# Kernel tuning notes

Measured on AMD Instinct MI355X. Metric: run time of the kernel, lower is better.

Reference implementation:

```python
import jax, jax.numpy as jnp
import numpy as np

D, H, HK, DH = 2048, 32, 8, 64
RQ = RKV = 48
RO = RFF = 1024
INTER = 8192
B, T = 2, 1024
THETA = 10000.0
EPS = 1e-5
NEG = -1e30


def _rms(x, w):
    v = jnp.mean(x * x, axis=-1, keepdims=True)
    return x * jax.lax.rsqrt(v + EPS) * w


def _proj_per_head(x, Us, V):
    # x:[B,T,D], V:[h,r,D], Us:[h,dh,r] -> [B,h,T,dh]
    xr = jnp.einsum('btd,hrd->bthr', x, V)
    return jnp.einsum('bthr,hdr->bhtd', xr, Us)


def _rope_cos_sin(position_ids, dh):
    inv = 1.0 / (THETA ** (jnp.arange(0, dh, 2, dtype=jnp.float32) / dh))
    ang = position_ids.astype(jnp.float32)[:, None] * inv[None, :]   # [T, dh/2]
    ang = jnp.repeat(ang, 2, axis=-1)                                # interleaved, per source
    return jnp.cos(ang), jnp.sin(ang)                                # [T, dh]


def _rotate_half(x):
    d = x.shape[-1] // 2
    return jnp.concatenate([-x[..., d:], x[..., :d]], axis=-1)


def setup_inputs() -> dict:
    key = jax.random.key(0)
    ks = jax.random.split(key, 18)
    g = lambda i, shape, s: (jax.random.normal(ks[i], shape, jnp.float32) * s)
    return {
        'x': g(0, (B, T, D), 1.0),
        'position_ids': jnp.arange(T, dtype=jnp.int32),
        'ln1_w': jnp.ones((D,), jnp.float32),
        'ln2_w': jnp.ones((D,), jnp.float32),
        'q_Us': g(1, (H, DH, RQ), 0.05), 'q_V': g(2, (H, RQ, D), 0.05),
        'k_Us': g(3, (HK, DH, RKV), 0.05), 'k_V': g(4, (HK, RKV, D), 0.05),
        'v_Us': g(5, (HK, DH, RKV), 0.05), 'v_V': g(6, (HK, RKV, D), 0.05),
        'o_Us': g(7, (D, RO), 0.02), 'o_V': g(8, (RO, H * DH), 0.02),
        'g_Us': g(9, (INTER, RFF), 0.02), 'g_V': g(10, (RFF, D), 0.02),
        'u_Us': g(11, (INTER, RFF), 0.02), 'u_V': g(12, (RFF, D), 0.02),
        'd_Us': g(13, (D, RFF), 0.02), 'd_V': g(14, (RFF, INTER), 0.02),
    }


def reference(x, position_ids, ln1_w, ln2_w,
              q_Us, q_V, k_Us, k_V, v_Us, v_V,
              o_Us, o_V, g_Us, g_V, u_Us, u_V, d_Us, d_V):
    Bx, Tx, Dx = x.shape
    n_rep = H // HK

    # ---- attention sub-block ----
    h = _rms(x, ln1_w)
    q = _proj_per_head(h, q_Us, q_V)          # [B,H,T,dh]
    k = _proj_per_head(h, k_Us, k_V)          # [B,Hk,T,dh]
    v = _proj_per_head(h, v_Us, v_V)          # [B,Hk,T,dh]

    cos, sin = _rope_cos_sin(position_ids, DH)          # [T,dh]
    cos = cos[None, None]; sin = sin[None, None]
    q = q * cos + _rotate_half(q) * sin
    k = k * cos + _rotate_half(k) * sin

    k = jnp.repeat(k, n_rep, axis=1)          # GQA expand -> [B,H,T,dh]
    v = jnp.repeat(v, n_rep, axis=1)

    scale = 1.0 / jnp.sqrt(jnp.float32(DH))
    scores = jnp.einsum('bhtd,bhsd->bhts', q, k) * scale
    causal = jnp.tril(jnp.ones((Tx, Tx), bool))
    scores = jnp.where(causal[None, None], scores, NEG)
    p = jax.nn.softmax(scores, axis=-1)
    attn = jnp.einsum('bhts,bhsd->bhtd', p, v)            # [B,H,T,dh]
    attn = attn.transpose(0, 2, 1, 3).reshape(Bx, Tx, H * DH)

    # low-rank o projection: W_o ~= o_Us @ o_V
    ar = jnp.einsum('btk,rk->btr', attn, o_V)
    attn_out = jnp.einsum('btr,dr->btd', ar, o_Us)
    x = x + attn_out

    # ---- low-rank SwiGLU MLP ----
    h2 = _rms(x, ln2_w)
    gate = jnp.einsum('btr,ir->bti', jnp.einsum('btd,rd->btr', h2, g_V), g_Us)
    up = jnp.einsum('btr,ir->bti', jnp.einsum('btd,rd->btr', h2, u_V), u_Us)
    inner = jax.nn.silu(gate) * up
    down = jnp.einsum('btr,dr->btd', jnp.einsum('bti,ri->btr', inner, d_V), d_Us)
    return x + down
```

## Files before the change

kernel.cpp:

```cpp
#include <hip/hip_runtime.h>

typedef unsigned short u16;
typedef unsigned int u32;
typedef unsigned long long u64;

typedef __bf16 bf16x8 __attribute__((ext_vector_type(8)));
typedef float f32x4 __attribute__((ext_vector_type(4)));

__device__ __forceinline__ float bf2f(u16 u) {
  union { u32 i; float f; } v; v.i = ((u32)u) << 16; return v.f;
}
__device__ __forceinline__ u16 f2bf(float f) {
  union { float f; u32 i; } v; v.f = f;
  u32 r = v.i + 0x7fff + ((v.i >> 16) & 1);
  return (u16)(r >> 16);
}
__device__ __forceinline__ u32 packbf(float a, float b) {
  return (u32)f2bf(a) | ((u32)f2bf(b) << 16);
}

__device__ __forceinline__ void gload_lds16(const u16* g, u16* l) {
  __builtin_amdgcn_global_load_lds(
      (const __attribute__((address_space(1))) void*)g,
      (__attribute__((address_space(3))) void*)l, 16, 0, 0);
}

__global__ void detect_k(const u32* __restrict__ w, u32* __restrict__ flag) {
  if (threadIdx.x == 0 && blockIdx.x == 0)
    *flag = (w[0] == 0x3F803F80u) ? 0u : 1u;
}

struct CvtTab {
  const void* src[16];
  u64 doff[16];
  u32 bstart[16];
};

__global__ __launch_bounds__(256)
void convert_k(CvtTab tab, u16* __restrict__ wbase, const u32* __restrict__ dflag)
{
  const u32 f = *dflag;
  const int blk = blockIdx.x;
  int t = 15;
#pragma unroll
  for (int i = 15; i >= 1; i--) if (blk < (int)tab.bstart[i]) t = i - 1;
  const u64 eoff = (u64)(blk - tab.bstart[t]) * 2048 + threadIdx.x * 8;
  u16* dst = wbase + tab.doff[t] + eoff;
  if (f == 0) {
    uint4 v = *(const uint4*)((const u16*)tab.src[t] + eoff);
    *(uint4*)dst = v;
  } else {
    const float* s = (const float*)tab.src[t] + eoff;
    uint4 lo = *(const uint4*)s;
    uint4 hi = *(const uint4*)(s + 4);
    union { u32 i; float fv; } c0,c1,c2,c3,c4,c5,c6,c7;
    c0.i = lo.x; c1.i = lo.y; c2.i = lo.z; c3.i = lo.w;
    c4.i = hi.x; c5.i = hi.y; c6.i = hi.z; c7.i = hi.w;
    uint4 pb;
    pb.x = packbf(c0.fv, c1.fv); pb.y = packbf(c2.fv, c3.fv);
    pb.z = packbf(c4.fv, c5.fv); pb.w = packbf(c6.fv, c7.fv);
    *(uint4*)dst = pb;
  }
}

template<int EPI, int TILE, int BK>
__global__ __launch_bounds__(256)
void gemm_bt(const u16* __restrict__ A, const u16* __restrict__ B,
             void* Cout, const void* R,
             int K, int lda, int ldc, int pstride, const u32* __restrict__ dflag)
{
  constexpr int WT = TILE / 2;
  constexpr int NF = TILE / 32;
  constexpr int CH = BK / 8;
  constexpr int ITER_S = TILE * CH / 256;
  __shared__ u16 sA[TILE * BK];
  __shared__ u16 sB[TILE * BK];
  const u32 f = *dflag;
  const int tid  = threadIdx.x;
  const int bm   = blockIdx.y * TILE;
  const int bn   = blockIdx.x * TILE;
  const int Klen = K / gridDim.z;
  const int kbase = blockIdx.z * Klen;
  const int wave = tid >> 6, lane = tid & 63;
  const int wm = (wave >> 1) * WT, wn = (wave & 1) * WT;
  const int lr = lane & 15, lq = lane >> 4;

  f32x4 acc[NF][NF];
#pragma unroll
  for (int i = 0; i < NF; i++)
#pragma unroll
    for (int j = 0; j < NF; j++) { f32x4 z = {0.f,0.f,0.f,0.f}; acc[i][j] = z; }

  int scA[ITER_S], scRow[ITER_S];
#pragma unroll
  for (int j = 0; j < ITER_S; j++) {
    int s = (wave * ITER_S + j) * 64 + lane;
    scRow[j] = s / CH;
    scA[j] = (((s % CH)) ^ (scRow[j] & 7)) * 8;
  }

  for (int k0 = kbase; k0 < kbase + Klen; k0 += BK) {
#pragma unroll
    for (int j = 0; j < ITER_S; j++) {
      const u16* ga = A + (size_t)(bm + scRow[j]) * lda + k0 + scA[j];
      const u16* gb = B + (size_t)(bn + scRow[j]) * K + k0 + scA[j];
      gload_lds16(ga, &sA[(wave * ITER_S + j) * 512]);
      gload_lds16(gb, &sB[(wave * ITER_S + j) * 512]);
    }
    __syncthreads();
#pragma unroll
    for (int kk = 0; kk < BK; kk += 32) {
      bf16x8 af[NF], bfr[NF];
#pragma unroll
      for (int i = 0; i < NF; i++)
        af[i] = *(const bf16x8*)
            &sA[(wm + i * 16 + lr) * BK + ((((kk >> 3) + lq) ^ (lr & 7)) * 8)];
#pragma unroll
      for (int i = 0; i < NF; i++)
        bfr[i] = *(const bf16x8*)
            &sB[(wn + i * 16 + lr) * BK + ((((kk >> 3) + lq) ^ (lr & 7)) * 8)];
#pragma unroll
      for (int i = 0; i < NF; i++)
#pragma unroll
        for (int j = 0; j < NF; j++)
          acc[i][j] = __builtin_amdgcn_mfma_f32_16x16x32_bf16(af[i], bfr[j], acc[i][j], 0, 0, 0);
    }
    __syncthreads();
  }

  u16* outz = (u16*)Cout + (size_t)blockIdx.z * pstride;
#pragma unroll
  for (int i = 0; i < NF; i++) {
#pragma unroll
    for (int j = 0; j < NF; j++) {
#pragma unroll
      for (int e = 0; e < 4; e++) {
        int row = bm + wm + i * 16 + lq * 4 + e;
        int col = bn + wn + j * 16 + lr;
        size_t idx = (size_t)row * ldc + col;
        float v = acc[i][j][e];
        if (EPI == 0) {
          outz[idx] = f2bf(v);
        } else if (EPI == 1) {
          float rv = f ? ((const float*)R)[idx] : bf2f(((const u16*)R)[idx]);
          ((float*)Cout)[idx] = v + rv;
        } else if (EPI == 2) {
          float s = v + ((const float*)R)[idx];
          if (f) ((float*)Cout)[idx] = s;
          else   ((u16*)Cout)[idx] = f2bf(s);
        }
      }
    }
  }
}

__global__ __launch_bounds__(256)
void gemm_gu(const u16* __restrict__ A, const u16* __restrict__ Bg,
             const u16* __restrict__ Bu, u16* __restrict__ Cout,
             int K, int lda, int ldc)
{
  constexpr int TILE = 128, BK = 64, NF = 4, CH = 8, ITER_S = 4;
  __shared__ u16 sA[TILE * BK];
  __shared__ u16 sB[TILE * BK];
  const int tid  = threadIdx.x;
  const int bm   = blockIdx.y * TILE;
  const int bn   = blockIdx.x * TILE;
  const int wave = tid >> 6, lane = tid & 63;
  const int wm = (wave >> 1) * 64, wn = (wave & 1) * 64;
  const int lr = lane & 15, lq = lane >> 4;

  f32x4 accG[NF][NF], accU[NF][NF];
#pragma unroll
  for (int i = 0; i < NF; i++)
#pragma unroll
    for (int j = 0; j < NF; j++) {
      f32x4 z = {0.f,0.f,0.f,0.f}; accG[i][j] = z; accU[i][j] = z;
    }

  int scA[ITER_S], scRow[ITER_S];
#pragma unroll
  for (int j = 0; j < ITER_S; j++) {
    int s = (wave * ITER_S + j) * 64 + lane;
    scRow[j] = s / CH;
    scA[j] = ((s % CH) ^ (scRow[j] & 7)) * 8;
  }

#pragma unroll
  for (int ph = 0; ph < 2; ph++) {
    const u16* Ap = A + (ph ? 1024 : 0);
    const u16* Bp = ph ? Bu : Bg;
    for (int k0 = 0; k0 < K; k0 += BK) {
#pragma unroll
      for (int j = 0; j < ITER_S; j++) {
        gload_lds16(Ap + (size_t)(bm + scRow[j]) * lda + k0 + scA[j],
                    &sA[(wave * ITER_S + j) * 512]);
        gload_lds16(Bp + (size_t)(bn + scRow[j]) * K + k0 + scA[j],
                    &sB[(wave * ITER_S + j) * 512]);
      }
      __syncthreads();
#pragma unroll
      for (int kk = 0; kk < BK; kk += 32) {
        bf16x8 af[NF], bfr[NF];
#pragma unroll
        for (int i = 0; i < NF; i++)
          af[i] = *(const bf16x8*)
              &sA[(wm + i * 16 + lr) * BK + ((((kk >> 3) + lq) ^ (lr & 7)) * 8)];
#pragma unroll
        for (int i = 0; i < NF; i++)
          bfr[i] = *(const bf16x8*)
              &sB[(wn + i * 16 + lr) * BK + ((((kk >> 3) + lq) ^ (lr & 7)) * 8)];
        if (ph == 0) {
#pragma unroll
          for (int i = 0; i < NF; i++)
#pragma unroll
            for (int j = 0; j < NF; j++)
              accG[i][j] = __builtin_amdgcn_mfma_f32_16x16x32_bf16(af[i], bfr[j], accG[i][j], 0, 0, 0);
        } else {
#pragma unroll
          for (int i = 0; i < NF; i++)
#pragma unroll
            for (int j = 0; j < NF; j++)
              accU[i][j] = __builtin_amdgcn_mfma_f32_16x16x32_bf16(af[i], bfr[j], accU[i][j], 0, 0, 0);
        }
      }
      __syncthreads();
    }
  }

#pragma unroll
  for (int i = 0; i < NF; i++) {
#pragma unroll
    for (int j = 0; j < NF; j++) {
#pragma unroll
      for (int e = 0; e < 4; e++) {
        int row = bm + wm + i * 16 + lq * 4 + e;
        int col = bn + wn + j * 16 + lr;
        float g = accG[i][j][e];
        float inner = g / (1.f + __expf(-g)) * accU[i][j][e];
        Cout[(size_t)row * ldc + col] = f2bf(inner);
      }
    }
  }
}

__global__ __launch_bounds__(256)
void reduce2_k(const u16* __restrict__ p, u16* __restrict__ out, int nel)
{
  size_t i = ((size_t)blockIdx.x * 256 + threadIdx.x) * 8;
  uint4 a = *(const uint4*)(p + i);
  uint4 b = *(const uint4*)(p + (size_t)nel + i);
  u32 aa[4] = {a.x, a.y, a.z, a.w};
  u32 bb[4] = {b.x, b.y, b.z, b.w};
  u32 rr[4];
#pragma unroll
  for (int k = 0; k < 4; k++) {
    float s0 = bf2f((u16)aa[k]) + bf2f((u16)bb[k]);
    float s1 = bf2f((u16)(aa[k] >> 16)) + bf2f((u16)(bb[k] >> 16));
    rr[k] = packbf(s0, s1);
  }
  uint4 o; o.x = rr[0]; o.y = rr[1]; o.z = rr[2]; o.w = rr[3];
  *(uint4*)(out + i) = o;
}

template<int XSRC>
__global__ __launch_bounds__(256)
void rmsnorm_k(const void* __restrict__ xin, const u16* __restrict__ w,
               u16* __restrict__ out, const u32* __restrict__ dflag)
{
  const u32 f = *dflag;
  const int n = blockIdx.x, tid = threadIdx.x;
  float v[8]; float ss = 0.f;
#pragma unroll
  for (int i = 0; i < 8; i++) {
    int d = i * 256 + tid;
    float xv;
    if (XSRC == 1)      xv = ((const float*)xin)[(size_t)n * 2048 + d];
    else if (f)         xv = ((const float*)xin)[(size_t)n * 2048 + d];
    else                xv = bf2f(((const u16*)xin)[(size_t)n * 2048 + d]);
    v[i] = xv; ss += xv * xv;
  }
#pragma unroll
  for (int o = 32; o >= 1; o >>= 1) ss += __shfl_xor(ss, o, 64);
  __shared__ float red[4];
  if ((tid & 63) == 0) red[tid >> 6] = ss;
  __syncthreads();
  float tot = red[0] + red[1] + red[2] + red[3];
  float rms = rsqrtf(tot * (1.f / 2048.f) + 1e-5f);
#pragma unroll
  for (int i = 0; i < 8; i++) {
    int d = i * 256 + tid;
    out[(size_t)n * 2048 + d] = f2bf(v[i] * rms * bf2f(w[d]));
  }
}

template<int ROPE, int TRANS>
__global__ __launch_bounds__(256)
void qkv2_k(const u16* __restrict__ xr, const u16* __restrict__ Us,
            const int* __restrict__ pos, u16* __restrict__ out, int NH, int XS)
{
  const int h = blockIdx.y;
  const int tid = threadIdx.x;
  const int n = blockIdx.x * 8 + (tid >> 5);
  const int j = tid & 31;
  const u16* xrow = xr + (size_t)n * XS + h * 48;
  const u16* U = Us + (size_t)h * 64 * 48;
  float a = 0.f, b = 0.f;
#pragma unroll
  for (int r = 0; r < 48; r++) {
    float xv = bf2f(xrow[r]);
    a += xv * bf2f(U[j * 48 + r]);
    b += xv * bf2f(U[(j + 32) * 48 + r]);
  }
  const int t = n & 1023, bb = n >> 10;
  float olo, ohi;
  if (ROPE) {
    float p = (float)pos[t];
    float inv_lo = powf(10000.f, -(float)(2 * (j >> 1)) * (1.f / 64.f));
    float inv_hi = powf(10000.f, -(float)(2 * (16 + (j >> 1))) * (1.f / 64.f));
    float sl, cl, sh, ch;
    sincosf(p * inv_lo, &sl, &cl);
    sincosf(p * inv_hi, &sh, &ch);
    olo = a * cl - b * sl;
    ohi = b * ch + a * sh;
  } else { olo = a; ohi = b; }
  if (TRANS == 0) {
    size_t ob = ((size_t)(bb * NH + h) * 1024 + t) * 64;
    out[ob + j] = f2bf(olo);
    out[ob + j + 32] = f2bf(ohi);
  } else {
    size_t ob = (size_t)(bb * NH + h) * 64 * 1024;
    out[ob + (size_t)j * 1024 + t] = f2bf(olo);
    out[ob + (size_t)(j + 32) * 1024 + t] = f2bf(ohi);
  }
}

__global__ __launch_bounds__(256)
void flash_k(const u16* __restrict__ Q, const u16* __restrict__ K,
             const u16* __restrict__ VT, u16* __restrict__ O)
{
  __shared__ u16 sQ[64 * 72];
  __shared__ u16 sK[128 * 72];
  __shared__ u16 sVT[64 * 136];
  __shared__ u16 sP[64 * 136];
  const int bh = blockIdx.x;
  const int b = bh >> 5, h = bh & 31, hk = h >> 2;
  const int t0 = blockIdx.y << 6;
  const int tid = threadIdx.x, wave = tid >> 6, lane = tid & 63;
  const int lr = lane & 15, lq = lane >> 4;
  const int qr = wave * 16;
  const size_t bhk = (size_t)(b * 8 + hk);
  const u16* Qb = Q + ((size_t)bh * 1024 + t0) * 64;
  const u16* Kb = K + bhk * 1024 * 64;
  const u16* Vb = VT + bhk * 64 * 1024;

#pragma unroll
  for (int i = 0; i < 2; i++) {
    int c = tid + i * 256;
    int row = c >> 3, col = (c & 7) * 8;
    *(uint4*)&sQ[row * 72 + col] = *(const uint4*)(Qb + row * 64 + col);
  }

  f32x4 acc[4];
#pragma unroll
  for (int dt = 0; dt < 4; dt++) { f32x4 z = {0.f,0.f,0.f,0.f}; acc[dt] = z; }
  float m[4], l[4];
#pragma unroll
  for (int e = 0; e < 4; e++) { m[e] = -3.0e38f; l[e] = 0.f; }

  const int ntiles = (t0 >> 7) + 1;
  for (int st = 0; st < ntiles; st++) {
    __syncthreads();
#pragma unroll
    for (int i = 0; i < 4; i++) {
      int c = tid + i * 256;
      int row = c >> 3, col = (c & 7) * 8;
      *(uint4*)&sK[row * 72 + col] =
          *(const uint4*)(Kb + (size_t)(st * 128 + row) * 64 + col);
    }
#pragma unroll
    for (int i = 0; i < 4; i++) {
      int c = tid + i * 256;
      int d = c >> 4, t8 = (c & 15) * 8;
      *(uint4*)&sVT[d * 136 + t8] =
          *(const uint4*)(Vb + (size_t)d * 1024 + st * 128 + t8);
    }
    __syncthreads();

    bf16x8 aq0 = *(const bf16x8*)&sQ[(qr + lr) * 72 + lq * 8];
    bf16x8 aq1 = *(const bf16x8*)&sQ[(qr + lr) * 72 + 32 + lq * 8];
    f32x4 sf[8];
#pragma unroll
    for (int nt = 0; nt < 8; nt++) {
      f32x4 z = {0.f,0.f,0.f,0.f};
      bf16x8 bk0 = *(const bf16x8*)&sK[(nt * 16 + lr) * 72 + lq * 8];
      bf16x8 bk1 = *(const bf16x8*)&sK[(nt * 16 + lr) * 72 + 32 + lq * 8];
      z = __builtin_amdgcn_mfma_f32_16x16x32_bf16(aq0, bk0, z, 0, 0, 0);
      z = __builtin_amdgcn_mfma_f32_16x16x32_bf16(aq1, bk1, z, 0, 0, 0);
      sf[nt] = z;
    }

    const int colbase = st * 128;
#pragma unroll
    for (int e = 0; e < 4; e++) {
      const int row = t0 + qr + lq * 4 + e;
      float tm = -3.0e38f;
#pragma unroll
      for (int nt = 0; nt < 8; nt++) {
        float v = sf[nt][e] * 0.125f;
        if (colbase + nt * 16 + lr > row) v = -1e30f;
        sf[nt][e] = v;
        tm = fmaxf(tm, v);
      }
      tm = fmaxf(tm, __shfl_xor(tm, 1, 64));
      tm = fmaxf(tm, __shfl_xor(tm, 2, 64));
      tm = fmaxf(tm, __shfl_xor(tm, 4, 64));
      tm = fmaxf(tm, __shfl_xor(tm, 8, 64));
      float mnew = fmaxf(m[e], tm);
      float alpha = __expf(m[e] - mnew);
      m[e] = mnew;
      float ts = 0.f;
#pragma unroll
      for (int nt = 0; nt < 8; nt++) {
        float p = __expf(sf[nt][e] - mnew);
        sP[(qr + lq * 4 + e) * 136 + nt * 16 + lr] = f2bf(p);
        ts += p;
      }
      ts += __shfl_xor(ts, 1, 64);
      ts += __shfl_xor(ts, 2, 64);
      ts += __shfl_xor(ts, 4, 64);
      ts += __shfl_xor(ts, 8, 64);
      l[e] = l[e] * alpha + ts;
#pragma unroll
      for (int dt = 0; dt < 4; dt++) acc[dt][e] *= alpha;
    }

#pragma unroll
    for (int kk = 0; kk < 4; kk++) {
      bf16x8 pa = *(const bf16x8*)&sP[(qr + lr) * 136 + kk * 32 + lq * 8];
#pragma unroll
      for (int dt = 0; dt < 4; dt++) {
        bf16x8 bv = *(const bf16x8*)&sVT[(dt * 16 + lr) * 136 + kk * 32 + lq * 8];
        acc[dt] = __builtin_amdgcn_mfma_f32_16x16x32_bf16(pa, bv, acc[dt], 0, 0, 0);
      }
    }
  }

#pragma unroll
  for (int e = 0; e < 4; e++) {
    float inv = 1.f / l[e];
    int t = t0 + qr + lq * 4 + e;
#pragma unroll
    for (int dt = 0; dt < 4; dt++) {
      size_t idx = ((size_t)(b * 1024 + t)) * 2048 + h * 64 + dt * 16 + lr;
      O[idx] = f2bf(acc[dt][e] * inv);
    }
  }
}

extern "C" void kernel_launch(void* const* d_in, const int* in_sizes, int n_in,
                              void* d_out, int out_size, void* d_ws, size_t ws_size,
                              hipStream_t stream)
{
  const void* x    = d_in[0];
  const int* pos   = (const int*)d_in[1];

  char* ws = (char*)d_ws;
  const size_t MB = 1048576;
  float* x1     = (float*)(ws + 0 * MB);
  u16*   gate   = (u16*)  (ws + 16 * MB);
  u16*   h1     = (u16*)  (ws + 16 * MB);
  u16*   attn   = (u16*)  (ws + 16 * MB);
  u16*   xr_all = (u16*)  (ws + 24 * MB);
  u16*   ar     = (u16*)  (ws + 24 * MB);
  u16*   h2     = (u16*)  (ws + 28 * MB);
  u16*   qb     = (u16*)  (ws + 33 * MB);
  u16*   kb     = (u16*)  (ws + 41 * MB);
  u16*   vbt    = (u16*)  (ws + 43 * MB);
  u16*   part   = (u16*)  (ws + 48 * MB);
  u16*   gr_ur  = (u16*)  (ws + 48 * MB);
  u16*   dr     = (u16*)  (ws + 56 * MB);
  u16*   wb     = (u16*)  (ws + 60 * MB);
  u32*   flag   = (u32*)  (ws + 60 * MB + 81043456);

  u16* wQKV = wb + 0;
  u16* wGU  = wb + 4718592;
  u16* oVc  = wb + 8912896;
  u16* oUsc = wb + 11010048;
  u16* gUsc = wb + 13107200;
  u16* uUsc = wb + 21495808;
  u16* dVc  = wb + 29884416;
  u16* dUsc = wb + 38273024;
  u16* qUsc = wb + 40370176;
  u16* kUsc = wb + 40468480;
  u16* vUsc = wb + 40493056;
  u16* ln1c = wb + 40517632;
  u16* ln2c = wb + 40519680;

  CvtTab tab;
  const int srcidx[16] = {5, 7, 9, 13, 15, 11, 10, 12, 14, 17, 16, 4, 6, 8, 2, 3};
  const u64 doff[16] = {0, 3145728, 3932160, 4718592, 6815744, 8912896, 11010048,
                        13107200, 21495808, 29884416, 38273024, 40370176,
                        40468480, 40493056, 40517632, 40519680};
  const u32 bstart[16] = {0, 1536, 1920, 2304, 3328, 4352, 5376, 6400, 10496,
                          14592, 18688, 19712, 19760, 19772, 19784, 19785};
  for (int i = 0; i < 16; i++) {
    tab.src[i] = d_in[srcidx[i]];
    tab.doff[i] = doff[i];
    tab.bstart[i] = bstart[i];
  }

  dim3 blk(256);
  const int PS = 2097152;

  detect_k<<<1, 64, 0, stream>>>((const u32*)d_in[2], flag);
  convert_k<<<19786, blk, 0, stream>>>(tab, wb, flag);

  rmsnorm_k<0><<<2048, blk, 0, stream>>>(x, ln1c, h1, flag);

  gemm_bt<0,64,128><<<dim3(36, 32), blk, 0, stream>>>(h1, wQKV, xr_all, nullptr,
                                                      2048, 2048, 2304, 0, flag);

  qkv2_k<1,0><<<dim3(256, 32), blk, 0, stream>>>(xr_all,        qUsc, pos, qb, 32, 2304);
  qkv2_k<1,0><<<dim3(256, 8),  blk, 0, stream>>>(xr_all + 1536, kUsc, pos, kb, 8,  2304);
  qkv2_k<0,1><<<dim3(256, 8),  blk, 0, stream>>>(xr_all + 1920, vUsc, pos, vbt, 8, 2304);

  flash_k<<<dim3(64, 16), blk, 0, stream>>>(qb, kb, vbt, attn);

  gemm_bt<0,64,128><<<dim3(16, 32, 2), blk, 0, stream>>>(attn, oVc, part, nullptr,
                                                         2048, 2048, 1024, PS, flag);
  reduce2_k<<<1024, blk, 0, stream>>>(part, ar, PS);
  gemm_bt<1,64,128><<<dim3(32, 32), blk, 0, stream>>>(ar, oUsc, x1, x,
                                                      1024, 1024, 2048, 0, flag);

  rmsnorm_k<1><<<2048, blk, 0, stream>>>(x1, ln2c, h2, flag);

  gemm_bt<0,64,128><<<dim3(32, 32), blk, 0, stream>>>(h2, wGU, gr_ur, nullptr,
                                                      2048, 2048, 2048, 0, flag);

  gemm_gu<<<dim3(64, 16), blk, 0, stream>>>(gr_ur, gUsc, uUsc, gate,
                                            1024, 2048, 8192);

  gemm_bt<0,64,128><<<dim3(16, 32, 2), blk, 0, stream>>>(gate, dVc, part, nullptr,
                                                         8192, 8192, 1024, PS, flag);
  reduce2_k<<<1024, blk, 0, stream>>>(part, dr, PS);
  gemm_bt<2,64,128><<<dim3(32, 32), blk, 0, stream>>>(dr, dUsc, d_out, x1,
                                                      1024, 1024, 2048, 0, flag);
}
```

Before: 591.7 us.

## Replace fused gate/up GEMM with pipelined 256x256-tile 8-wave GEMM pair

Replaces the 128x128 gate/up kernel, which ran both phases in one block, with a 512-thread, 256x256-tile GEMM that double-buffers LDS and overlaps global-to-LDS loads with MFMA in four quadrant sub-steps, using setprio and explicit barriers. It is launched twice. The first launch writes silu(gate) to the output buffer, and the second multiplies the up projection into it in place. The aim is more data reuse per tile and better overlap of memory and compute. In exchange, the intermediate makes an extra bf16 round trip through memory, gate is rounded to bf16 before the multiply, and the grid drops to 256 blocks.

```diff
diff --git a/kernel.cpp b/kernel.cpp
--- a/kernel.cpp
+++ b/kernel.cpp
@@ -154,90 +154,165 @@
   }
 }
 
-__global__ __launch_bounds__(256)
-void gemm_gu(const u16* __restrict__ A, const u16* __restrict__ Bg,
-             const u16* __restrict__ Bu, u16* __restrict__ Cout,
-             int K, int lda, int ldc)
-{
-  constexpr int TILE = 128, BK = 64, NF = 4, CH = 8, ITER_S = 4;
-  __shared__ u16 sA[TILE * BK];
-  __shared__ u16 sB[TILE * BK];
-  const int tid  = threadIdx.x;
-  const int bm   = blockIdx.y * TILE;
-  const int bn   = blockIdx.x * TILE;
+template<int EPI>
+__global__ __launch_bounds__(512, 2)
+void gemm8_k(const u16* __restrict__ A, const u16* __restrict__ B,
+             u16* C, const u16* R,
+             int K, int lda, int ldb, int ldc)
+{
+  __shared__ __align__(16) u16 lds[2][2][2][8192];
+  const int tid = threadIdx.x;
   const int wave = tid >> 6, lane = tid & 63;
-  const int wm = (wave >> 1) * 64, wn = (wave & 1) * 64;
+  const int bm = blockIdx.y << 8, bn = blockIdx.x << 8;
+  const int wr = wave >> 2, wc = wave & 3;
   const int lr = lane & 15, lq = lane >> 4;
-
-  f32x4 accG[NF][NF], accU[NF][NF];
-#pragma unroll
-  for (int i = 0; i < NF; i++)
-#pragma unroll
-    for (int j = 0; j < NF; j++) {
-      f32x4 z = {0.f,0.f,0.f,0.f}; accG[i][j] = z; accU[i][j] = z;
-    }
-
-  int scA[ITER_S], scRow[ITER_S];
-#pragma unroll
-  for (int j = 0; j < ITER_S; j++) {
-    int s = (wave * ITER_S + j) * 64 + lane;
-    scRow[j] = s / CH;
-    scA[j] = ((s % CH) ^ (scRow[j] & 7)) * 8;
-  }
-
-#pragma unroll
-  for (int ph = 0; ph < 2; ph++) {
-    const u16* Ap = A + (ph ? 1024 : 0);
-    const u16* Bp = ph ? Bu : Bg;
-    for (int k0 = 0; k0 < K; k0 += BK) {
-#pragma unroll
-      for (int j = 0; j < ITER_S; j++) {
-        gload_lds16(Ap + (size_t)(bm + scRow[j]) * lda + k0 + scA[j],
-                    &sA[(wave * ITER_S + j) * 512]);
-        gload_lds16(Bp + (size_t)(bn + scRow[j]) * K + k0 + scA[j],
-                    &sB[(wave * ITER_S + j) * 512]);
-      }
-      __syncthreads();
-#pragma unroll
-      for (int kk = 0; kk < BK; kk += 32) {
-        bf16x8 af[NF], bfr[NF];
-#pragma unroll
-        for (int i = 0; i < NF; i++)
-          af[i] = *(const bf16x8*)
-              &sA[(wm + i * 16 + lr) * BK + ((((kk >> 3) + lq) ^ (lr & 7)) * 8)];
-#pragma unroll
-        for (int i = 0; i < NF; i++)
-          bfr[i] = *(const bf16x8*)
-              &sB[(wn + i * 16 + lr) * BK + ((((kk >> 3) + lq) ^ (lr & 7)) * 8)];
-        if (ph == 0) {
-#pragma unroll
-          for (int i = 0; i < NF; i++)
-#pragma unroll
-            for (int j = 0; j < NF; j++)
-              accG[i][j] = __builtin_amdgcn_mfma_f32_16x16x32_bf16(af[i], bfr[j], accG[i][j], 0, 0, 0);
+  const int NT = K >> 6;
+
+  int srow[2], skoff[2], soff[2];
+#pragma unroll
+  for (int j = 0; j < 2; j++) {
+    int seg = wave * 2 + j;
+    int s = seg * 64 + lane;
+    srow[j] = s >> 3;
+    skoff[j] = ((s & 7) ^ (srow[j] & 7)) * 8;
+    soff[j] = seg * 512;
+  }
+
+  auto STAGE = [&](int pb, int mat, int half, int kt) {
+    const u16* G = mat ? B : A;
+    const int ldg = mat ? ldb : lda;
+    const int r0 = (mat ? bn : bm) + half * 128;
+#pragma unroll
+    for (int j = 0; j < 2; j++)
+      gload_lds16(G + (size_t)(r0 + srow[j]) * ldg + (kt << 6) + skoff[j],
+                  &lds[pb][mat][half][soff[j]]);
+  };
+
+  f32x4 acc[8][4];
+#pragma unroll
+  for (int i = 0; i < 8; i++)
+#pragma unroll
+    for (int j = 0; j < 4; j++) { f32x4 z = {0.f,0.f,0.f,0.f}; acc[i][j] = z; }
+
+  int koff[2];
+  koff[0] = ((0 + lq) ^ (lr & 7)) * 8;
+  koff[1] = ((4 + lq) ^ (lr & 7)) * 8;
+  const int brow = (wc & 1) * 64;
+
+  STAGE(0, 0, 0, 0); STAGE(0, 1, 0, 0); STAGE(0, 1, 1, 0); STAGE(0, 0, 1, 0);
+  STAGE(1, 0, 0, 1); STAGE(1, 1, 0, 1); STAGE(1, 1, 1, 1);
+  asm volatile("s_waitcnt vmcnt(6)" ::: "memory");
+  __builtin_amdgcn_s_barrier();
+
+  for (int t = 0; t < NT; ++t) {
+    const int p = t & 1, pn = p ^ 1;
+    int s1 = t + 1; if (s1 >= NT) s1 -= NT;
+    int s2 = t + 2; if (s2 >= NT) s2 -= NT;
+    const u16* lA = &lds[p][0][wr][0];
+    const u16* lB = &lds[p][1][wc >> 1][0];
+    bf16x8 aF[8][2], bF[4][2];
+
+#pragma unroll
+    for (int fi = 0; fi < 4; fi++)
+#pragma unroll
+      for (int ks = 0; ks < 2; ks++)
+        aF[fi][ks] = *(const bf16x8*)&lA[(fi * 16 + lr) * 64 + koff[ks]];
+#pragma unroll
+    for (int fj = 0; fj < 2; fj++)
+#pragma unroll
+      for (int ks = 0; ks < 2; ks++)
+        bF[fj][ks] = *(const bf16x8*)&lB[(brow + fj * 16 + lr) * 64 + koff[ks]];
+    STAGE(pn, 0, 1, s1);
+    __builtin_amdgcn_s_barrier();
+    asm volatile("s_waitcnt lgkmcnt(0)" ::: "memory");
+    __builtin_amdgcn_sched_barrier(0);
+    __builtin_amdgcn_s_setprio(1);
+#pragma unroll
+    for (int ii = 0; ii < 4; ii++)
+#pragma unroll
+      for (int jj = 0; jj < 2; jj++)
+#pragma unroll
+        for (int ks = 0; ks < 2; ks++)
+          acc[ii][jj] = __builtin_amdgcn_mfma_f32_16x16x32_bf16(
+              aF[ii][ks], bF[jj][ks], acc[ii][jj], 0, 0, 0);
+    __builtin_amdgcn_s_setprio(0);
+    __builtin_amdgcn_s_barrier();
+
+#pragma unroll
+    for (int fi = 0; fi < 4; fi++)
+#pragma unroll
+      for (int ks = 0; ks < 2; ks++)
+        aF[4 + fi][ks] = *(const bf16x8*)&lA[((4 + fi) * 16 + lr) * 64 + koff[ks]];
+#pragma unroll
+    for (int fj = 0; fj < 2; fj++)
+#pragma unroll
+      for (int ks = 0; ks < 2; ks++)
+        bF[2 + fj][ks] = *(const bf16x8*)&lB[(brow + (2 + fj) * 16 + lr) * 64 + koff[ks]];
+    __builtin_amdgcn_s_barrier();
+    asm volatile("s_waitcnt lgkmcnt(0)" ::: "memory");
+    __builtin_amdgcn_sched_barrier(0);
+    __builtin_amdgcn_s_setprio(1);
+#pragma unroll
+    for (int ii = 0; ii < 4; ii++)
+#pragma unroll
+      for (int jj = 0; jj < 2; jj++)
+#pragma unroll
+        for (int ks = 0; ks < 2; ks++)
+          acc[4 + ii][2 + jj] = __builtin_amdgcn_mfma_f32_16x16x32_bf16(
+              aF[4 + ii][ks], bF[2 + jj][ks], acc[4 + ii][2 + jj], 0, 0, 0);
+    __builtin_amdgcn_s_setprio(0);
+    __builtin_amdgcn_s_barrier();
+
+    STAGE(p, 0, 0, s2);
+    STAGE(p, 1, 0, s2);
+    __builtin_amdgcn_s_barrier();
+    __builtin_amdgcn_s_setprio(1);
+#pragma unroll
+    for (int ii = 0; ii < 4; ii++)
+#pragma unroll
+      for (int jj = 0; jj < 2; jj++)
+#pragma unroll
+        for (int ks = 0; ks < 2; ks++)
+          acc[4 + ii][jj] = __builtin_amdgcn_mfma_f32_16x16x32_bf16(
+              aF[4 + ii][ks], bF[jj][ks], acc[4 + ii][jj], 0, 0, 0);
+    __builtin_amdgcn_s_setprio(0);
+    __builtin_amdgcn_s_barrier();
+
+    STAGE(p, 1, 1, s2);
+    __builtin_amdgcn_s_barrier();
+    __builtin_amdgcn_s_setprio(1);
+#pragma unroll
+    for (int ii = 0; ii < 4; ii++)
+#pragma unroll
+      for (int jj = 0; jj < 2; jj++)
+#pragma unroll
+        for (int ks = 0; ks < 2; ks++)
+          acc[ii][2 + jj] = __builtin_amdgcn_mfma_f32_16x16x32_bf16(
+              aF[ii][ks], bF[2 + jj][ks], acc[ii][2 + jj], 0, 0, 0);
+    __builtin_amdgcn_s_setprio(0);
+    asm volatile("s_waitcnt vmcnt(6)" ::: "memory");
+    __builtin_amdgcn_s_barrier();
+  }
+
+  asm volatile("s_waitcnt vmcnt(0)" ::: "memory");
+
+  const int orow0 = bm + wr * 128 + lq * 4;
+  const int ocol0 = bn + wc * 64 + lr;
+#pragma unroll
+  for (int i = 0; i < 8; i++) {
+#pragma unroll
+    for (int j = 0; j < 4; j++) {
+#pragma unroll
+      for (int e = 0; e < 4; e++) {
+        int row = orow0 + i * 16 + e;
+        int col = ocol0 + j * 16;
+        size_t idx = (size_t)row * ldc + col;
+        float v = acc[i][j][e];
+        if (EPI == 0) {
+          C[idx] = f2bf(v / (1.f + __expf(-v)));
         } else {
-#pragma unroll
-          for (int i = 0; i < NF; i++)
-#pragma unroll
-            for (int j = 0; j < NF; j++)
-              accU[i][j] = __builtin_amdgcn_mfma_f32_16x16x32_bf16(af[i], bfr[j], accU[i][j], 0, 0, 0);
+          C[idx] = f2bf(bf2f(R[idx]) * v);
         }
-      }
-      __syncthreads();
-    }
-  }
-
-#pragma unroll
-  for (int i = 0; i < NF; i++) {
-#pragma unroll
-    for (int j = 0; j < NF; j++) {
-#pragma unroll
-      for (int e = 0; e < 4; e++) {
-        int row = bm + wm + i * 16 + lq * 4 + e;
-        int col = bn + wn + j * 16 + lr;
-        float g = accG[i][j][e];
-        float inner = g / (1.f + __expf(-g)) * accU[i][j][e];
-        Cout[(size_t)row * ldc + col] = f2bf(inner);
       }
     }
   }
@@ -537,8 +612,10 @@
   gemm_bt<0,64,128><<<dim3(32, 32), blk, 0, stream>>>(h2, wGU, gr_ur, nullptr,
                                                       2048, 2048, 2048, 0, flag);
 
-  gemm_gu<<<dim3(64, 16), blk, 0, stream>>>(gr_ur, gUsc, uUsc, gate,
-                                            1024, 2048, 8192);
+  gemm8_k<0><<<dim3(32, 8), dim3(512), 0, stream>>>(gr_ur, gUsc, gate, nullptr,
+                                                    1024, 2048, 1024, 8192);
+  gemm8_k<1><<<dim3(32, 8), dim3(512), 0, stream>>>(gr_ur + 1024, uUsc, gate, gate,
+                                                    1024, 2048, 1024, 8192);
 
   gemm_bt<0,64,128><<<dim3(16, 32, 2), blk, 0, stream>>>(gate, dVc, part, nullptr,
                                                          8192, 8192, 1024, PS, flag);
```

Measured after the change: 609.7 us. 1.03x slower.
